# Kernel tuning notes

Hardware: AMD Instinct MI355X
Metric: run time of the kernel (lower is better)

The kernel has to match this reference:

```python
import jax, jax.numpy as jnp
import numpy as np

B, I, N, D = 4, 32, 4096, 64
TEM = 1.0
WP = 0.5


def setup_inputs() -> dict:
    key = jax.random.key(0)
    kf, kl = jax.random.split(key)
    x = jax.random.normal(kf, (B, N, D), dtype=jnp.float32)
    # features are L2-normalized ('normed_corr_features')
    x = x / jnp.linalg.norm(x, axis=-1, keepdims=True)
    # assign each correspondence to one of I instances -> boolean masks [B, I, N]
    inst = jax.random.randint(kl, (B, N), 0, I)
    label = (inst[:, None, :] == jnp.arange(I)[None, :, None])  # bool [B, I, N]
    return {"normed_corr_features": x, "label": label}


def reference(normed_corr_features, label):
    x = normed_corr_features                      # [B, N, D]
    m = label.astype(x.dtype)                     # [B, I, N]
    cnt = m.sum(-1)                               # [B, I]
    valid = (cnt >= 5).astype(x.dtype)            # skip instances with <5 points

    sim = jnp.einsum('bpd,bnd->bpn', x, x)        # [B, N, N] full similarity

    # loss_p: mse(sim_p, ones) over the cnt x cnt masked submatrix
    sq = (sim - 1.0) ** 2                         # [B, N, N]
    t = jnp.einsum('bip,bpn->bin', m, sq)         # [B, I, N]
    lp = (t * m).sum(-1) / jnp.maximum(cnt * cnt, 1.0)  # [B, I]

    # loss_n: mean over positive rows p of log(sum over negatives n of exp(sim/tem))
    e = jnp.exp(sim / TEM)                        # [B, N, N]
    s = jnp.einsum('bpn,bin->bip', e, 1.0 - m)    # [B, I, N] row sums over negatives
    ln = (jnp.log(jnp.maximum(s, 1e-30)) * m).sum(-1) / jnp.maximum(cnt, 1.0)  # [B, I]

    denom = jnp.asarray(B * I, x.dtype)
    loss_p = (valid * lp).sum() / denom
    loss_n = (valid * ln).sum() / denom
    return WP * loss_p + (1.0 - WP) * loss_n
```

## Files before the change

### kernel.cpp

```cpp
#include <hip/hip_runtime.h>
#include <stdint.h>

#define Bsz 4
#define Isz 32
#define Nsz 4096
#define Dsz 64
#define WPc 0.5f
#define ALPHA 1.2011224087864498f
#define LN2 0.69314718055994531f
#define LSZ2 256
#define GBLK (Isz * Bsz * 2)

typedef __attribute__((ext_vector_type(8))) short short8;
typedef __attribute__((ext_vector_type(4))) float floatx4;

__device__ inline uint16_t f2bf(float f) {
  uint32_t u = __float_as_uint(f);
  u += 0x7fffu + ((u >> 16) & 1u);
  return (uint16_t)(u >> 16);
}
__device__ inline float exp2_raw(float f) { return __builtin_amdgcn_exp2f(f); }

__global__ __launch_bounds__(256) void prep_kernel(
    const float* __restrict__ x, uint16_t* __restrict__ xb,
    uint4* __restrict__ xbf, float* __restrict__ negtot,
    float* __restrict__ accum, int* __restrict__ ticket) {
  const int t = threadIdx.x;
  const int blk = blockIdx.x;
  const int idx4 = (blk * 256 + t) * 4;
  const float4 v = *(const float4*)(x + idx4);
  ushort4 o;
  o.x = f2bf(v.x * ALPHA);
  o.y = f2bf(v.y * ALPHA);
  o.z = f2bf(v.z * ALPHA);
  o.w = f2bf(v.w * ALPHA);
  *(ushort4*)(xb + idx4) = o;

  if (blk < 512) {
    const int gid = blk * 256 + t;
    const int lane = gid & 63;
    const int kh = (gid >> 6) & 1;
    const int tile_g = gid >> 7;
    const int m = lane & 15;
    const int quad = lane >> 4;
    const size_t src = (size_t)(tile_g * 16 + m) * Dsz + kh * 32 + quad * 8;
    const float4 a = *(const float4*)(x + src);
    const float4 c = *(const float4*)(x + src + 4);
    ushort4 lo, hi;
    lo.x = f2bf(a.x * ALPHA); lo.y = f2bf(a.y * ALPHA);
    lo.z = f2bf(a.z * ALPHA); lo.w = f2bf(a.w * ALPHA);
    hi.x = f2bf(c.x * ALPHA); hi.y = f2bf(c.y * ALPHA);
    hi.z = f2bf(c.z * ALPHA); hi.w = f2bf(c.w * ALPHA);
    ushort4* dst = (ushort4*)(xbf + gid);
    dst[0] = lo;
    dst[1] = hi;
  }
  if (blk < 64) {
    const int p = blk * 256 + t;
    negtot[p] = 0.f;
    if (p == 0) {
      accum[0] = 0.f;
      ticket[0] = 0;
    }
  }
}

__global__ __launch_bounds__(256) void rowsum5_kernel(
    const uint4* __restrict__ xbf, float* __restrict__ negtot) {
  const int t = threadIdx.x;
  const int lane = t & 63;
  const int w = t >> 6;
  const int quad = lane >> 4;
  const int l15 = lane & 15;

  const int b = blockIdx.y;
  const int rt0 = (blockIdx.x >> 3) * 8;
  const int ct0 = (blockIdx.x & 7) * 32;
  const int tb = b * 256;

  short8 af[2][2];
#pragma unroll
  for (int rt = 0; rt < 2; ++rt) {
    const int tile = tb + rt0 + w * 2 + rt;
#pragma unroll
    for (int kh = 0; kh < 2; ++kh)
      af[rt][kh] = *(const short8*)&xbf[(size_t)(tile * 2 + kh) * 64 + lane];
  }

  float negAll[2][4] = {{0.f, 0.f, 0.f, 0.f}, {0.f, 0.f, 0.f, 0.f}};

#pragma unroll 1
  for (int cg = 0; cg < 8; ++cg) {
    short8 bf[4][2];
#pragma unroll
    for (int ci = 0; ci < 4; ++ci) {
      const int tile = tb + ct0 + cg * 4 + ci;
#pragma unroll
      for (int kh = 0; kh < 2; ++kh)
        bf[ci][kh] = *(const short8*)&xbf[(size_t)(tile * 2 + kh) * 64 + lane];
    }
    floatx4 acc[2][4];
#pragma unroll
    for (int rt = 0; rt < 2; ++rt)
#pragma unroll
      for (int ci = 0; ci < 4; ++ci) acc[rt][ci] = (floatx4){0.f, 0.f, 0.f, 0.f};
#pragma unroll
    for (int kh = 0; kh < 2; ++kh)
#pragma unroll
      for (int ci = 0; ci < 4; ++ci)
#pragma unroll
        for (int rt = 0; rt < 2; ++rt)
          acc[rt][ci] = __builtin_amdgcn_mfma_f32_16x16x32_bf16(
              af[rt][kh], bf[ci][kh], acc[rt][ci], 0, 0, 0);
#pragma unroll
    for (int ci = 0; ci < 4; ++ci)
#pragma unroll
      for (int rt = 0; rt < 2; ++rt)
#pragma unroll
        for (int r = 0; r < 4; ++r) negAll[rt][r] += exp2_raw(acc[rt][ci][r]);
  }

  const size_t bN = (size_t)b * Nsz;
  const int wrow0 = rt0 * 16 + w * 32;
#pragma unroll
  for (int rt = 0; rt < 2; ++rt)
#pragma unroll
    for (int r = 0; r < 4; ++r) {
      float g = negAll[rt][r];
#pragma unroll
      for (int m = 1; m < 16; m <<= 1) g += __shfl_xor(g, m, 64);
      if (l15 == 0)
        atomicAdd(&negtot[bN + wrow0 + rt * 16 + quad * 4 + r], g);
    }
}

__global__ __launch_bounds__(256) void gram2_kernel(
    const uint16_t* __restrict__ xb, const uint8_t* __restrict__ label,
    const float* __restrict__ negtot, float* __restrict__ accum,
    int* __restrict__ ticket, float* __restrict__ out) {
  __shared__ int list[LSZ2];
  __shared__ int scnt;
  __shared__ uint4 grow[LSZ2 * 8];
  __shared__ float sPos[4];
  __shared__ float sLn[4];

  const int t = threadIdx.x;
  const int lane = t & 63;
  const int w = t >> 6;
  const int quad = lane >> 4;
  const int l15 = lane & 15;
  const int i = blockIdx.x;
  const int b = blockIdx.y;
  const int rc = blockIdx.z;
  const size_t bN = (size_t)b * Nsz;
  const uint16_t* xbB = xb + bN * Dsz;

  if (t == 0) scnt = 0;
  __syncthreads();
  {
    const uint4 lv = ((const uint4*)(label + ((size_t)b * Isz + i) * Nsz))[t];
    const uint32_t words[4] = {lv.x, lv.y, lv.z, lv.w};
#pragma unroll
    for (int jw = 0; jw < 4; ++jw)
#pragma unroll
      for (int jb = 0; jb < 4; ++jb) {
        if ((words[jw] >> (jb * 8)) & 0xff) {
          const int idx = atomicAdd(&scnt, 1);
          if (idx < LSZ2) list[idx] = t * 16 + jw * 4 + jb;
        }
      }
  }
  __syncthreads();
  const int cnt = scnt;
  const int cntE = cnt < LSZ2 ? cnt : LSZ2;

  for (int s = t; s < cntE * 8; s += 256) {
    const int j = s >> 3, u = s & 7;
    grow[(j << 3) | (u ^ (j & 7))] =
        *(const uint4*)(xbB + (size_t)list[j] * Dsz + u * 8);
  }
  __syncthreads();

  const bool active = (cnt >= 5) && (rc * 128 < cntE);
  if (active) {
    short8 af[2][2];
#pragma unroll
    for (int rt = 0; rt < 2; ++rt) {
      int ridx = rc * 128 + w * 32 + rt * 16 + l15;
      ridx = ridx < cntE ? ridx : cntE - 1;
#pragma unroll
      for (int kh = 0; kh < 2; ++kh) {
        const int u = quad + kh * 4;
        af[rt][kh] = *(const short8*)&grow[(ridx << 3) | (u ^ (ridx & 7))];
      }
    }

    float pos = 0.f, lns = 0.f;
    float ngrow_acc[2][4] = {{0.f, 0.f, 0.f, 0.f}, {0.f, 0.f, 0.f, 0.f}};
    const int nch = (cntE + 127) >> 7;
    for (int cc = 0; cc < nch; ++cc) {
      short8 bfr[8][2];
      bool cvalid[8];
#pragma unroll
      for (int ct = 0; ct < 8; ++ct) {
        const int cidx0 = cc * 128 + ct * 16 + l15;
        const int cidx = cidx0 < cntE ? cidx0 : cntE - 1;
        cvalid[ct] = cidx0 < cntE;
#pragma unroll
        for (int kh = 0; kh < 2; ++kh) {
          const int u = quad + kh * 4;
          bfr[ct][kh] = *(const short8*)&grow[(cidx << 3) | (u ^ (cidx & 7))];
        }
      }
      floatx4 acc[2][8];
#pragma unroll
      for (int rt = 0; rt < 2; ++rt)
#pragma unroll
        for (int ct = 0; ct < 8; ++ct) acc[rt][ct] = (floatx4){0.f, 0.f, 0.f, 0.f};
#pragma unroll
      for (int kh = 0; kh < 2; ++kh)
#pragma unroll
        for (int ct = 0; ct < 8; ++ct)
#pragma unroll
          for (int rt = 0; rt < 2; ++rt)
            acc[rt][ct] = __builtin_amdgcn_mfma_f32_16x16x32_bf16(
                af[rt][kh], bfr[ct][kh], acc[rt][ct], 0, 0, 0);
#pragma unroll
      for (int rt = 0; rt < 2; ++rt) {
        const int rbase = rc * 128 + w * 32 + rt * 16 + quad * 4;
#pragma unroll
        for (int ct = 0; ct < 8; ++ct) {
#pragma unroll
          for (int r = 0; r < 4; ++r) {
            const bool ok = cvalid[ct] && (rbase + r < cntE);
            const float s = acc[rt][ct][r];
            const float d = __builtin_fmaf(s, LN2, -1.f);
            pos += ok ? d * d : 0.f;
            ngrow_acc[rt][r] += ok ? exp2_raw(s) : 0.f;
          }
        }
      }
    }
#pragma unroll
    for (int rt = 0; rt < 2; ++rt)
#pragma unroll
      for (int r = 0; r < 4; ++r) {
        float g = ngrow_acc[rt][r];
#pragma unroll
        for (int m = 1; m < 16; m <<= 1) g += __shfl_xor(g, m, 64);
        const int ridx = rc * 128 + w * 32 + rt * 16 + quad * 4 + r;
        if (l15 == 0 && ridx < cntE) {
          const float nf = negtot[bN + list[ridx]] - g;
          lns += __logf(fmaxf(nf, 1e-30f));
        }
      }
#pragma unroll
    for (int m = 1; m < 64; m <<= 1) {
      pos += __shfl_xor(pos, m, 64);
      lns += __shfl_xor(lns, m, 64);
    }
    if (lane == 0) {
      sPos[w] = pos;
      sLn[w] = lns;
    }
    __syncthreads();
    if (t == 0) {
      const float pt = sPos[0] + sPos[1] + sPos[2] + sPos[3];
      const float lt = sLn[0] + sLn[1] + sLn[2] + sLn[3];
      const float c = (float)cnt;
      atomicAdd(accum, WPc * pt / (c * c) + (1.f - WPc) * lt / c);
    }
  }
  if (t == 0) {
    __threadfence();
    const int old = atomicAdd(ticket, 1);
    if (old == GBLK - 1) {
      const float tot = atomicAdd(accum, 0.f);
      out[0] = tot / (float)(Bsz * Isz);
    }
  }
}

extern "C" void kernel_launch(void* const* d_in, const int* in_sizes, int n_in,
                              void* d_out, int out_size, void* d_ws,
                              size_t ws_size, hipStream_t stream) {
  const float* x = (const float*)d_in[0];
  const uint8_t* label = (const uint8_t*)d_in[1];
  float* out = (float*)d_out;

  uint16_t* xb = (uint16_t*)d_ws;
  uint4* xbf = (uint4*)(xb + (size_t)Bsz * Nsz * Dsz);
  float* negtot = (float*)(xbf + (size_t)Bsz * Nsz * Dsz / 8);
  float* accum = negtot + Bsz * Nsz;
  int* ticket = (int*)(accum + 1);

  prep_kernel<<<(Bsz * Nsz * Dsz) / (256 * 4), 256, 0, stream>>>(
      x, xb, xbf, negtot, accum, ticket);

  dim3 gridA(256, Bsz);
  rowsum5_kernel<<<gridA, 256, 0, stream>>>(xbf, negtot);

  dim3 gridB(Isz, Bsz, 2);
  gram2_kernel<<<gridB, 256, 0, stream>>>(xb, label, negtot, accum, ticket, out);
}
```

Measured before the change: 89.09 us.

## Drop row-major bf16 copy and retile rowsum per-wave to 4x2 tile blocks

The prep kernel now writes only the MFMA fragment-layout bf16 buffer, and gram2 gathers rows from that layout through index arithmetic. This removes the second bf16 copy and its writes. The rowsum kernel gives each wave its own 4 row tiles against 16 column tiles, loading 2 column tiles per step, which changes the A/B register reuse ratio. It also adds a launch_bounds occupancy hint. In exchange, gram2's gather becomes a more scattered read from the fragment layout.

```diff
diff --git a/kernel.cpp b/kernel.cpp
--- a/kernel.cpp
+++ b/kernel.cpp
@@ -22,50 +22,36 @@
 __device__ inline float exp2_raw(float f) { return __builtin_amdgcn_exp2f(f); }
 
 __global__ __launch_bounds__(256) void prep_kernel(
-    const float* __restrict__ x, uint16_t* __restrict__ xb,
-    uint4* __restrict__ xbf, float* __restrict__ negtot,
-    float* __restrict__ accum, int* __restrict__ ticket) {
-  const int t = threadIdx.x;
-  const int blk = blockIdx.x;
-  const int idx4 = (blk * 256 + t) * 4;
-  const float4 v = *(const float4*)(x + idx4);
-  ushort4 o;
-  o.x = f2bf(v.x * ALPHA);
-  o.y = f2bf(v.y * ALPHA);
-  o.z = f2bf(v.z * ALPHA);
-  o.w = f2bf(v.w * ALPHA);
-  *(ushort4*)(xb + idx4) = o;
-
-  if (blk < 512) {
-    const int gid = blk * 256 + t;
-    const int lane = gid & 63;
-    const int kh = (gid >> 6) & 1;
-    const int tile_g = gid >> 7;
-    const int m = lane & 15;
-    const int quad = lane >> 4;
-    const size_t src = (size_t)(tile_g * 16 + m) * Dsz + kh * 32 + quad * 8;
-    const float4 a = *(const float4*)(x + src);
-    const float4 c = *(const float4*)(x + src + 4);
-    ushort4 lo, hi;
-    lo.x = f2bf(a.x * ALPHA); lo.y = f2bf(a.y * ALPHA);
-    lo.z = f2bf(a.z * ALPHA); lo.w = f2bf(a.w * ALPHA);
-    hi.x = f2bf(c.x * ALPHA); hi.y = f2bf(c.y * ALPHA);
-    hi.z = f2bf(c.z * ALPHA); hi.w = f2bf(c.w * ALPHA);
-    ushort4* dst = (ushort4*)(xbf + gid);
-    dst[0] = lo;
-    dst[1] = hi;
-  }
-  if (blk < 64) {
-    const int p = blk * 256 + t;
-    negtot[p] = 0.f;
-    if (p == 0) {
+    const float* __restrict__ x, uint4* __restrict__ xbf,
+    float* __restrict__ negtot, float* __restrict__ accum,
+    int* __restrict__ ticket) {
+  const int gid = blockIdx.x * 256 + threadIdx.x;
+  const int m = gid & 15;
+  const int quad = (gid >> 4) & 3;
+  const int kh = (gid >> 6) & 1;
+  const int tile_g = gid >> 7;
+  const size_t src = (size_t)(tile_g * 16 + m) * Dsz + kh * 32 + quad * 8;
+  const float4 a = *(const float4*)(x + src);
+  const float4 c = *(const float4*)(x + src + 4);
+  ushort4 lo, hi;
+  lo.x = f2bf(a.x * ALPHA); lo.y = f2bf(a.y * ALPHA);
+  lo.z = f2bf(a.z * ALPHA); lo.w = f2bf(a.w * ALPHA);
+  hi.x = f2bf(c.x * ALPHA); hi.y = f2bf(c.y * ALPHA);
+  hi.z = f2bf(c.z * ALPHA); hi.w = f2bf(c.w * ALPHA);
+  ushort4* dst = (ushort4*)(xbf + gid);
+  dst[0] = lo;
+  dst[1] = hi;
+
+  if (blockIdx.x < 64) {
+    negtot[gid] = 0.f;
+    if (gid == 0) {
       accum[0] = 0.f;
       ticket[0] = 0;
     }
   }
 }
 
-__global__ __launch_bounds__(256) void rowsum5_kernel(
+__global__ __launch_bounds__(256, 4) void rowsum6_kernel(
     const uint4* __restrict__ xbf, float* __restrict__ negtot) {
   const int t = threadIdx.x;
   const int lane = t & 63;
@@ -74,68 +60,73 @@
   const int l15 = lane & 15;
 
   const int b = blockIdx.y;
-  const int rt0 = (blockIdx.x >> 3) * 8;
-  const int ct0 = (blockIdx.x & 7) * 32;
+  const int gw = blockIdx.x * 4 + w;
+  const int rg = gw >> 4;
+  const int cg = gw & 15;
   const int tb = b * 256;
 
-  short8 af[2][2];
-#pragma unroll
-  for (int rt = 0; rt < 2; ++rt) {
-    const int tile = tb + rt0 + w * 2 + rt;
+  short8 af[4][2];
+#pragma unroll
+  for (int i = 0; i < 4; ++i) {
+    const int tile = tb + rg * 4 + i;
 #pragma unroll
     for (int kh = 0; kh < 2; ++kh)
-      af[rt][kh] = *(const short8*)&xbf[(size_t)(tile * 2 + kh) * 64 + lane];
-  }
-
-  float negAll[2][4] = {{0.f, 0.f, 0.f, 0.f}, {0.f, 0.f, 0.f, 0.f}};
+      af[i][kh] = *(const short8*)&xbf[(size_t)(tile * 2 + kh) * 64 + lane];
+  }
+
+  float negAll[4][4];
+#pragma unroll
+  for (int i = 0; i < 4; ++i)
+#pragma unroll
+    for (int r = 0; r < 4; ++r) negAll[i][r] = 0.f;
 
 #pragma unroll 1
-  for (int cg = 0; cg < 8; ++cg) {
-    short8 bf[4][2];
-#pragma unroll
-    for (int ci = 0; ci < 4; ++ci) {
-      const int tile = tb + ct0 + cg * 4 + ci;
+  for (int g = 0; g < 8; ++g) {
+    short8 bf[2][2];
+#pragma unroll
+    for (int c = 0; c < 2; ++c) {
+      const int tile = tb + cg * 16 + g * 2 + c;
 #pragma unroll
       for (int kh = 0; kh < 2; ++kh)
-        bf[ci][kh] = *(const short8*)&xbf[(size_t)(tile * 2 + kh) * 64 + lane];
-    }
-    floatx4 acc[2][4];
-#pragma unroll
-    for (int rt = 0; rt < 2; ++rt)
-#pragma unroll
-      for (int ci = 0; ci < 4; ++ci) acc[rt][ci] = (floatx4){0.f, 0.f, 0.f, 0.f};
+        bf[c][kh] = *(const short8*)&xbf[(size_t)(tile * 2 + kh) * 64 + lane];
+    }
+    floatx4 acc[4][2];
+#pragma unroll
+    for (int i = 0; i < 4; ++i)
+#pragma unroll
+      for (int c = 0; c < 2; ++c) acc[i][c] = (floatx4){0.f, 0.f, 0.f, 0.f};
 #pragma unroll
     for (int kh = 0; kh < 2; ++kh)
 #pragma unroll
-      for (int ci = 0; ci < 4; ++ci)
-#pragma unroll
-        for (int rt = 0; rt < 2; ++rt)
-          acc[rt][ci] = __builtin_amdgcn_mfma_f32_16x16x32_bf16(
-              af[rt][kh], bf[ci][kh], acc[rt][ci], 0, 0, 0);
-#pragma unroll
-    for (int ci = 0; ci < 4; ++ci)
-#pragma unroll
-      for (int rt = 0; rt < 2; ++rt)
-#pragma unroll
-        for (int r = 0; r < 4; ++r) negAll[rt][r] += exp2_raw(acc[rt][ci][r]);
+      for (int c = 0; c < 2; ++c)
+#pragma unroll
+        for (int i = 0; i < 4; ++i)
+          acc[i][c] = __builtin_amdgcn_mfma_f32_16x16x32_bf16(
+              af[i][kh], bf[c][kh], acc[i][c], 0, 0, 0);
+#pragma unroll
+    for (int c = 0; c < 2; ++c)
+#pragma unroll
+      for (int i = 0; i < 4; ++i)
+#pragma unroll
+        for (int r = 0; r < 4; ++r) negAll[i][r] += exp2_raw(acc[i][c][r]);
   }
 
   const size_t bN = (size_t)b * Nsz;
-  const int wrow0 = rt0 * 16 + w * 32;
-#pragma unroll
-  for (int rt = 0; rt < 2; ++rt)
+  const int wrow0 = rg * 64;
+#pragma unroll
+  for (int i = 0; i < 4; ++i)
 #pragma unroll
     for (int r = 0; r < 4; ++r) {
-      float g = negAll[rt][r];
+      float g = negAll[i][r];
 #pragma unroll
       for (int m = 1; m < 16; m <<= 1) g += __shfl_xor(g, m, 64);
       if (l15 == 0)
-        atomicAdd(&negtot[bN + wrow0 + rt * 16 + quad * 4 + r], g);
+        atomicAdd(&negtot[bN + wrow0 + i * 16 + quad * 4 + r], g);
     }
 }
 
 __global__ __launch_bounds__(256) void gram2_kernel(
-    const uint16_t* __restrict__ xb, const uint8_t* __restrict__ label,
+    const uint4* __restrict__ xbf, const uint8_t* __restrict__ label,
     const float* __restrict__ negtot, float* __restrict__ accum,
     int* __restrict__ ticket, float* __restrict__ out) {
   __shared__ int list[LSZ2];
@@ -153,7 +144,7 @@
   const int b = blockIdx.y;
   const int rc = blockIdx.z;
   const size_t bN = (size_t)b * Nsz;
-  const uint16_t* xbB = xb + bN * Dsz;
+  const int tb = b * 256;
 
   if (t == 0) scnt = 0;
   __syncthreads();
@@ -176,8 +167,10 @@
 
   for (int s = t; s < cntE * 8; s += 256) {
     const int j = s >> 3, u = s & 7;
-    grow[(j << 3) | (u ^ (j & 7))] =
-        *(const uint4*)(xbB + (size_t)list[j] * Dsz + u * 8);
+    const int p = list[j];
+    const size_t unit =
+        (size_t)((tb + (p >> 4)) * 2 + (u >> 2)) * 64 + (u & 3) * 16 + (p & 15);
+    grow[(j << 3) | (u ^ (j & 7))] = xbf[unit];
   }
   __syncthreads();
 
@@ -288,18 +281,16 @@
   const uint8_t* label = (const uint8_t*)d_in[1];
   float* out = (float*)d_out;
 
-  uint16_t* xb = (uint16_t*)d_ws;
-  uint4* xbf = (uint4*)(xb + (size_t)Bsz * Nsz * Dsz);
+  uint4* xbf = (uint4*)d_ws;
   float* negtot = (float*)(xbf + (size_t)Bsz * Nsz * Dsz / 8);
   float* accum = negtot + Bsz * Nsz;
   int* ticket = (int*)(accum + 1);
 
-  prep_kernel<<<(Bsz * Nsz * Dsz) / (256 * 4), 256, 0, stream>>>(
-      x, xb, xbf, negtot, accum, ticket);
+  prep_kernel<<<512, 256, 0, stream>>>(x, xbf, negtot, accum, ticket);
 
   dim3 gridA(256, Bsz);
-  rowsum5_kernel<<<gridA, 256, 0, stream>>>(xbf, negtot);
+  rowsum6_kernel<<<gridA, 256, 0, stream>>>(xbf, negtot);
 
   dim3 gridB(Isz, Bsz, 2);
-  gram2_kernel<<<gridB, 256, 0, stream>>>(xb, label, negtot, accum, ticket, out);
-}
+  gram2_kernel<<<gridB, 256, 0, stream>>>(xbf, label, negtot, accum, ticket, out);
+}
```

Measured after the change: 84.39 us. -5.3%, faster.
